# Kernel tuning notes

Measured on AMD Instinct MI355X. Metric: run time of the kernel, lower is better.

The kernel has to match this reference:

```python
import jax, jax.numpy as jnp
import numpy as np

N_NODES = 100000
N_EDGES = 800000
DIM = 64
HEADS = 4
HEAD_DIM = DIM // HEADS  # 16
ALPHA = 0.1
K_ITERS = 8  # fixed-point iterations approximating the implicit/CG solve


def setup_inputs() -> dict:
    key = jax.random.key(0)
    ks = jax.random.split(key, 7)
    x = jax.random.normal(ks[0], (N_NODES, DIM), dtype=jnp.float32)
    edge_index = jax.random.randint(ks[1], (2, N_EDGES), 0, N_NODES, dtype=jnp.int64)
    edge_attr = jax.random.normal(ks[2], (N_EDGES, DIM), dtype=jnp.float32)
    s = 1.0 / np.sqrt(DIM)
    Wq = jax.random.normal(ks[3], (DIM, DIM), dtype=jnp.float32) * s
    Wk = jax.random.normal(ks[4], (DIM, DIM), dtype=jnp.float32) * s
    Wv = jax.random.normal(ks[5], (DIM, DIM), dtype=jnp.float32) * s
    We = jax.random.normal(ks[6], (DIM, DIM), dtype=jnp.float32) * s
    return {"x": x, "edge_index": edge_index, "edge_attr": edge_attr,
            "Wq": Wq, "Wk": Wk, "Wv": Wv, "We": We}


def _mapr(x, edge_index, edge_attr, Wq, Wk, Wv, We):
    N = x.shape[0]
    src, dst = edge_index[0], edge_index[1]
    q = (x @ Wq).reshape(N, HEADS, HEAD_DIM)
    k = (x @ Wk).reshape(N, HEADS, HEAD_DIM)
    v = (x @ Wv).reshape(N, HEADS, HEAD_DIM)
    e = (edge_attr @ We).reshape(-1, HEADS, HEAD_DIM)
    # per-edge multi-head dot attention logits, edge features modulate keys
    logits = jnp.sum(q[dst] * (k[src] + e), axis=-1) / np.sqrt(HEAD_DIM)  # [E,H]
    # segment softmax over incoming edges of each dst node
    m = jax.ops.segment_max(logits, dst, num_segments=N)  # [N,H]
    ex = jnp.exp(logits - m[dst])
    denom = jax.ops.segment_sum(ex, dst, num_segments=N)  # [N,H]
    att = ex / (denom[dst] + 1e-16)  # [E,H]
    # implicit propagation: fixed-point solve of z = alpha*v + (1-alpha) * A_att z
    def step(z, _):
        msg = att[:, :, None] * z[src]                       # [E,H,D]
        agg = jax.ops.segment_sum(msg, dst, num_segments=N)  # [N,H,D]
        return ALPHA * v + (1.0 - ALPHA) * agg, None
    z, _ = jax.lax.scan(step, v, None, length=K_ITERS)
    return z.reshape(N, DIM)


def reference(x, edge_index, edge_attr, Wq, Wk, Wv, We):
    h = _mapr(x, edge_index, edge_attr, Wq, Wk, Wv, We)
    h = jax.nn.relu(h)  # act; dropout is identity in eval mode
    return x + h        # residual
```

## Files before the change

### kernel.cpp

```cpp
#include <hip/hip_runtime.h>
#include <hip/hip_fp16.h>
#include <cstdint>
#include <cstddef>

#define NN 100000
#define NE 800000
#define DIM 64
#define HEADS 4
#define HEAD_DIM 16
#define ALPHA 0.1f
#define K_ITERS 8
#define NBLK 391

typedef short bf16x8 __attribute__((ext_vector_type(8)));
typedef float f32x4 __attribute__((ext_vector_type(4)));

__device__ __forceinline__ unsigned short f2bf(float f) {
    unsigned int x = __float_as_uint(f);
    unsigned int r = (x + 0x7fffu + ((x >> 16) & 1u)) >> 16;
    return (unsigned short)r;
}
__device__ __forceinline__ float bf_lo(unsigned int p) { return __uint_as_float(p << 16); }
__device__ __forceinline__ float bf_hi(unsigned int p) { return __uint_as_float(p & 0xffff0000u); }

__device__ __forceinline__ float2 h2f(unsigned int v) {
    __half2 h = *(__half2*)&v;
    return __half22float2(h);
}
__device__ __forceinline__ unsigned int f2h2(float a, float b) {
    __half2 h = __floats2half2_rn(a, b);
    return *(unsigned int*)&h;
}
__device__ __forceinline__ float dot8h(uint4 a, uint4 b) {
    float2 a0 = h2f(a.x), b0 = h2f(b.x);
    float2 a1 = h2f(a.y), b1 = h2f(b.y);
    float2 a2 = h2f(a.z), b2 = h2f(b.z);
    float2 a3 = h2f(a.w), b3 = h2f(b.w);
    return a0.x * b0.x + a0.y * b0.y + a1.x * b1.x + a1.y * b1.y
         + a2.x * b2.x + a2.y * b2.y + a3.x * b3.x + a3.y * b3.y;
}

#define ACC8(a, V) { float2 t_; \
    t_ = h2f((V).x); m[0] += (a) * t_.x; m[1] += (a) * t_.y; \
    t_ = h2f((V).y); m[2] += (a) * t_.x; m[3] += (a) * t_.y; \
    t_ = h2f((V).z); m[4] += (a) * t_.x; m[5] += (a) * t_.y; \
    t_ = h2f((V).w); m[6] += (a) * t_.x; m[7] += (a) * t_.y; }

__global__ __launch_bounds__(256) void qkv_mfma_kernel(
    const float* __restrict__ x,
    const float* __restrict__ Wq, const float* __restrict__ Wk,
    const float* __restrict__ Wv, const float* __restrict__ We,
    __half* __restrict__ qh, __half* __restrict__ kh, __half* __restrict__ vh,
    unsigned short* __restrict__ u)
{
    __shared__ unsigned short sq[64 * 72];
    int tid = threadIdx.x;
    int w = tid >> 6;
    int lane = tid & 63;
    int m16 = lane & 15;
    int quad = lane >> 4;
    int node = blockIdx.x * 64 + w * 16 + m16;
    int nodeC = node < NN ? node : NN - 1;

    bf16x8 afrag[2];
    #pragma unroll
    for (int kk = 0; kk < 2; ++kk) {
        const float* xr = x + (size_t)nodeC * DIM + kk * 32 + quad * 8;
        #pragma unroll
        for (int j = 0; j < 8; ++j) afrag[kk][j] = (short)f2bf(xr[j]);
    }

    const float* Ws[3] = {Wq, Wk, Wv};
    __half* outs[3] = {qh, kh, vh};

    #pragma unroll
    for (int mtx = 0; mtx < 3; ++mtx) {
        const float* W = Ws[mtx];
        #pragma unroll
        for (int n0 = 0; n0 < 64; n0 += 16) {
            int col = n0 + m16;
            f32x4 acc = {0.f, 0.f, 0.f, 0.f};
            #pragma unroll
            for (int kk = 0; kk < 2; ++kk) {
                bf16x8 bfrag;
                #pragma unroll
                for (int j = 0; j < 8; ++j)
                    bfrag[j] = (short)f2bf(W[(kk * 32 + quad * 8 + j) * DIM + col]);
                acc = __builtin_amdgcn_mfma_f32_16x16x32_bf16(afrag[kk], bfrag, acc, 0, 0, 0);
            }
            if (mtx == 0) {
                #pragma unroll
                for (int r = 0; r < 4; ++r) acc[r] *= 0.25f;
            }
            #pragma unroll
            for (int r = 0; r < 4; ++r) {
                int rl = w * 16 + quad * 4 + r;
                int gnode = blockIdx.x * 64 + rl;
                if (mtx == 0) sq[rl * 72 + col] = f2bf(acc[r]);
                if (gnode < NN) outs[mtx][(size_t)gnode * DIM + col] = __float2half(acc[r]);
            }
        }
    }
    __syncthreads();

    #pragma unroll
    for (int h = 0; h < HEADS; ++h) {
        int kk = h >> 1;
        bf16x8 aq;
        const unsigned short* sr = &sq[(w * 16 + m16) * 72 + kk * 32 + quad * 8];
        #pragma unroll
        for (int j = 0; j < 8; ++j) aq[j] = (short)sr[j];
        #pragma unroll
        for (int c0 = 0; c0 < 64; c0 += 16) {
            int c = c0 + m16;
            bf16x8 bfrag;
            #pragma unroll
            for (int j = 0; j < 8; ++j) {
                int k = kk * 32 + quad * 8 + j;
                bfrag[j] = ((k >> 4) == h) ? (short)f2bf(We[c * DIM + k]) : (short)0;
            }
            f32x4 acc = {0.f, 0.f, 0.f, 0.f};
            acc = __builtin_amdgcn_mfma_f32_16x16x32_bf16(aq, bfrag, acc, 0, 0, 0);
            #pragma unroll
            for (int r = 0; r < 4; ++r) {
                int gnode = blockIdx.x * 64 + w * 16 + quad * 4 + r;
                if (gnode < NN) u[(size_t)gnode * 256 + h * 64 + c] = f2bf(acc[r]);
            }
        }
    }
}

__global__ void init_kernel(float* __restrict__ denom, int* __restrict__ deg) {
    int i = blockIdx.x * 256 + threadIdx.x;
    if (i < NN * HEADS) denom[i] = 0.f;
    if (i < NN) deg[i] = 0;
}

__global__ void deg_kernel(const int* __restrict__ ei, int* __restrict__ deg) {
    int e = blockIdx.x * 256 + threadIdx.x;
    if (e >= NE) return;
    atomicAdd(&deg[ei[NE + e]], 1);
}

__global__ void blocksum_kernel(const int* __restrict__ deg, int* __restrict__ bsum) {
    int t = threadIdx.x, b = blockIdx.x;
    int idx = b * 256 + t;
    int v = (idx < NN) ? deg[idx] : 0;
    #pragma unroll
    for (int off = 32; off > 0; off >>= 1) v += __shfl_down(v, off);
    __shared__ int wsum[4];
    if ((t & 63) == 0) wsum[t >> 6] = v;
    __syncthreads();
    if (t == 0) bsum[b] = wsum[0] + wsum[1] + wsum[2] + wsum[3];
}

__global__ void bscan_kernel(const int* __restrict__ bsum, int* __restrict__ boff) {
    __shared__ int s[512];
    int t = threadIdx.x;
    int v = (t < NBLK) ? bsum[t] : 0;
    s[t] = v;
    __syncthreads();
    for (int off = 1; off < 512; off <<= 1) {
        int u = (t >= off) ? s[t - off] : 0;
        __syncthreads();
        s[t] += u;
        __syncthreads();
    }
    if (t < NBLK) boff[t] = s[t] - v;
}

__global__ void rowptr_kernel(const int* __restrict__ deg, const int* __restrict__ boff,
                              int* __restrict__ row_ptr, int* __restrict__ cursor) {
    __shared__ int s[256];
    int t = threadIdx.x, b = blockIdx.x;
    int idx = b * 256 + t;
    int v = (idx < NN) ? deg[idx] : 0;
    s[t] = v;
    __syncthreads();
    for (int off = 1; off < 256; off <<= 1) {
        int u = (t >= off) ? s[t - off] : 0;
        __syncthreads();
        s[t] += u;
        __syncthreads();
    }
    if (idx < NN) {
        int ex = boff[b] + s[t] - v;
        row_ptr[idx] = ex;
        cursor[idx] = ex;
    }
    if (idx == 0) row_ptr[NN] = NE;
}

__global__ void scatter_kernel(const int* __restrict__ ei,
                               int* __restrict__ cursor,
                               int* __restrict__ csr_src,
                               int* __restrict__ csr_e,
                               int* __restrict__ csr_dst) {
    int e = blockIdx.x * 256 + threadIdx.x;
    if (e >= NE) return;
    int src = ei[e], dst = ei[NE + e];
    int pos = atomicAdd(&cursor[dst], 1);
    csr_src[pos] = src;
    csr_e[pos] = e;
    csr_dst[pos] = dst;
}

__global__ void logits_csr_kernel(const __half* __restrict__ qh,
                                  const __half* __restrict__ kh,
                                  const float* __restrict__ edge_attr,
                                  const unsigned short* __restrict__ u,
                                  const int* __restrict__ csr_src,
                                  const int* __restrict__ csr_e,
                                  const int* __restrict__ csr_dst,
                                  __half* __restrict__ att,
                                  float* __restrict__ denom) {
    int idx = blockIdx.x * 256 + threadIdx.x;
    if (idx >= NE * HEADS) return;
    int j = idx >> 2, h = idx & 3;
    int src = csr_src[j], dst = csr_dst[j], e = csr_e[j];
    const float4* attr4 = (const float4*)edge_attr + (size_t)e * 16;
    const uint4* u4 = (const uint4*)u + (size_t)dst * 32 + h * 8;
    float au = 0.f;
    #pragma unroll
    for (int i = 0; i < 8; ++i) {
        uint4 up = u4[i];
        float4 a0 = attr4[2 * i];
        float4 a1 = attr4[2 * i + 1];
        au += a0.x * bf_lo(up.x) + a0.y * bf_hi(up.x)
            + a0.z * bf_lo(up.y) + a0.w * bf_hi(up.y)
            + a1.x * bf_lo(up.z) + a1.y * bf_hi(up.z)
            + a1.z * bf_lo(up.w) + a1.w * bf_hi(up.w);
    }
    const uint4* qq = (const uint4*)qh + (size_t)dst * 8 + h * 2;
    const uint4* kk = (const uint4*)kh + (size_t)src * 8 + h * 2;
    float qk = dot8h(qq[0], kk[0]) + dot8h(qq[1], kk[1]);
    float ex = __expf(qk + au);
    att[idx] = __float2half(ex);
    atomicAdd(&denom[dst * HEADS + h], ex);
}

__global__ void prop_csr_kernel(const __half* __restrict__ zin,
                                const __half* __restrict__ vh,
                                const __half* __restrict__ att,
                                const int* __restrict__ csr_src,
                                const int* __restrict__ row_ptr,
                                const float* __restrict__ denom,
                                __half* __restrict__ zout) {
    int gid = blockIdx.x * 256 + threadIdx.x;
    int node = gid >> 3;
    if (node >= NN) return;
    int l = gid & 7;
    int head = l >> 1;
    const uint4* z4 = (const uint4*)zin;
    float m[8];
    #pragma unroll
    for (int i = 0; i < 8; ++i) m[i] = 0.f;
    int beg = row_ptr[node], end = row_ptr[node + 1];
    int j = beg;
    for (; j + 4 <= end; j += 4) {
        int s0 = csr_src[j], s1 = csr_src[j + 1], s2 = csr_src[j + 2], s3 = csr_src[j + 3];
        float a0 = __half2float(att[4 * j + head]);
        float a1 = __half2float(att[4 * j + 4 + head]);
        float a2 = __half2float(att[4 * j + 8 + head]);
        float a3 = __half2float(att[4 * j + 12 + head]);
        uint4 z0 = z4[(size_t)s0 * 8 + l];
        uint4 z1 = z4[(size_t)s1 * 8 + l];
        uint4 z2 = z4[(size_t)s2 * 8 + l];
        uint4 z3 = z4[(size_t)s3 * 8 + l];
        ACC8(a0, z0); ACC8(a1, z1); ACC8(a2, z2); ACC8(a3, z3);
    }
    for (; j < end; ++j) {
        int s = csr_src[j];
        float a = __half2float(att[4 * j + head]);
        uint4 zl = z4[(size_t)s * 8 + l];
        ACC8(a, zl);
    }
    float r = 0.9f / (denom[node * HEADS + head] + 1e-16f);
    uint4 vv = ((const uint4*)vh)[(size_t)node * 8 + l];
    float2 v0 = h2f(vv.x), v1 = h2f(vv.y), v2 = h2f(vv.z), v3 = h2f(vv.w);
    uint4 o;
    o.x = f2h2(ALPHA * v0.x + r * m[0], ALPHA * v0.y + r * m[1]);
    o.y = f2h2(ALPHA * v1.x + r * m[2], ALPHA * v1.y + r * m[3]);
    o.z = f2h2(ALPHA * v2.x + r * m[4], ALPHA * v2.y + r * m[5]);
    o.w = f2h2(ALPHA * v3.x + r * m[6], ALPHA * v3.y + r * m[7]);
    ((uint4*)zout)[(size_t)node * 8 + l] = o;
}

__global__ void prop_out_kernel(const __half* __restrict__ zin,
                                const __half* __restrict__ vh,
                                const __half* __restrict__ att,
                                const int* __restrict__ csr_src,
                                const int* __restrict__ row_ptr,
                                const float* __restrict__ denom,
                                const float* __restrict__ x,
                                float* __restrict__ out) {
    int gid = blockIdx.x * 256 + threadIdx.x;
    int node = gid >> 3;
    if (node >= NN) return;
    int l = gid & 7;
    int head = l >> 1;
    const uint4* z4 = (const uint4*)zin;
    float m[8];
    #pragma unroll
    for (int i = 0; i < 8; ++i) m[i] = 0.f;
    int beg = row_ptr[node], end = row_ptr[node + 1];
    int j = beg;
    for (; j + 4 <= end; j += 4) {
        int s0 = csr_src[j], s1 = csr_src[j + 1], s2 = csr_src[j + 2], s3 = csr_src[j + 3];
        float a0 = __half2float(att[4 * j + head]);
        float a1 = __half2float(att[4 * j + 4 + head]);
        float a2 = __half2float(att[4 * j + 8 + head]);
        float a3 = __half2float(att[4 * j + 12 + head]);
        uint4 z0 = z4[(size_t)s0 * 8 + l];
        uint4 z1 = z4[(size_t)s1 * 8 + l];
        uint4 z2 = z4[(size_t)s2 * 8 + l];
        uint4 z3 = z4[(size_t)s3 * 8 + l];
        ACC8(a0, z0); ACC8(a1, z1); ACC8(a2, z2); ACC8(a3, z3);
    }
    for (; j < end; ++j) {
        int s = csr_src[j];
        float a = __half2float(att[4 * j + head]);
        uint4 zl = z4[(size_t)s * 8 + l];
        ACC8(a, zl);
    }
    float r = 0.9f / (denom[node * HEADS + head] + 1e-16f);
    uint4 vv = ((const uint4*)vh)[(size_t)node * 8 + l];
    float2 v0 = h2f(vv.x), v1 = h2f(vv.y), v2 = h2f(vv.z), v3 = h2f(vv.w);
    float zf[8] = { ALPHA * v0.x + r * m[0], ALPHA * v0.y + r * m[1],
                    ALPHA * v1.x + r * m[2], ALPHA * v1.y + r * m[3],
                    ALPHA * v2.x + r * m[4], ALPHA * v2.y + r * m[5],
                    ALPHA * v3.x + r * m[6], ALPHA * v3.y + r * m[7] };
    const float4* x4 = (const float4*)x + (size_t)node * 16 + l * 2;
    float4 xa = x4[0], xb = x4[1];
    float4 oa, ob;
    oa.x = xa.x + fmaxf(zf[0], 0.f); oa.y = xa.y + fmaxf(zf[1], 0.f);
    oa.z = xa.z + fmaxf(zf[2], 0.f); oa.w = xa.w + fmaxf(zf[3], 0.f);
    ob.x = xb.x + fmaxf(zf[4], 0.f); ob.y = xb.y + fmaxf(zf[5], 0.f);
    ob.z = xb.z + fmaxf(zf[6], 0.f); ob.w = xb.w + fmaxf(zf[7], 0.f);
    float4* o4 = (float4*)out + (size_t)node * 16 + l * 2;
    o4[0] = oa; o4[1] = ob;
}

extern "C" void kernel_launch(void* const* d_in, const int* in_sizes, int n_in,
                              void* d_out, int out_size, void* d_ws, size_t ws_size,
                              hipStream_t stream) {
    const float* x         = (const float*)d_in[0];
    const int*   ei        = (const int*)d_in[1];
    const float* edge_attr = (const float*)d_in[2];
    const float* Wq        = (const float*)d_in[3];
    const float* Wk        = (const float*)d_in[4];
    const float* Wv        = (const float*)d_in[5];
    const float* We        = (const float*)d_in[6];
    float* out = (float*)d_out;

    __half* qh = (__half*)d_ws;
    __half* kh = qh + (size_t)NN * DIM;
    __half* vh = kh + (size_t)NN * DIM;
    unsigned short* u = (unsigned short*)(vh + (size_t)NN * DIM);
    __half* zha = (__half*)(u + (size_t)NN * 256);
    __half* zhb = zha + (size_t)NN * DIM;
    __half* att = zhb + (size_t)NN * DIM;
    float* denom = (float*)(att + (size_t)NE * HEADS);
    int* deg     = (int*)(denom + (size_t)NN * HEADS);
    int* bsum    = deg + NN;
    int* boff    = bsum + NBLK;
    int* row_ptr = boff + NBLK;
    int* cursor  = row_ptr + NN + 1;
    int* csr_src = cursor + NN;
    int* csr_e   = csr_src + NE;
    int* csr_dst = csr_e + NE;

    hipLaunchKernelGGL(qkv_mfma_kernel, dim3((NN + 63) / 64), dim3(256), 0, stream,
                       x, Wq, Wk, Wv, We, qh, kh, vh, u);
    hipLaunchKernelGGL(init_kernel, dim3((NN * HEADS + 255) / 256), dim3(256), 0, stream,
                       denom, deg);
    hipLaunchKernelGGL(deg_kernel, dim3((NE + 255) / 256), dim3(256), 0, stream,
                       ei, deg);
    hipLaunchKernelGGL(blocksum_kernel, dim3(NBLK), dim3(256), 0, stream,
                       deg, bsum);
    hipLaunchKernelGGL(bscan_kernel, dim3(1), dim3(512), 0, stream,
                       bsum, boff);
    hipLaunchKernelGGL(rowptr_kernel, dim3(NBLK), dim3(256), 0, stream,
                       deg, boff, row_ptr, cursor);
    hipLaunchKernelGGL(scatter_kernel, dim3((NE + 255) / 256), dim3(256), 0, stream,
                       ei, cursor, csr_src, csr_e, csr_dst);
    hipLaunchKernelGGL(logits_csr_kernel, dim3(NE * HEADS / 256), dim3(256), 0, stream,
                       qh, kh, edge_attr, u, csr_src, csr_e, csr_dst, att, denom);

    const __half* zin = vh;
    __half* zout = zha;
    for (int it = 0; it < K_ITERS - 1; ++it) {
        hipLaunchKernelGGL(prop_csr_kernel, dim3((NN * 8 + 255) / 256), dim3(256), 0, stream,
                           zin, vh, att, csr_src, row_ptr, denom, zout);
        zin = zout;
        zout = (zout == zha) ? zhb : zha;
    }
    hipLaunchKernelGGL(prop_out_kernel, dim3((NN * 8 + 255) / 256), dim3(256), 0, stream,
                       zin, vh, att, csr_src, row_ptr, denom, x, out);
}
```

Measured before the change: 734.9 us.

## Pack normalized attention and src into per-edge CSR records, drop denom atomics

Logits are now computed in original edge order, so edge_attr streams coalesced with nontemporal loads, and the per-edge atomicAdd into denom is removed. A per-node kernel sums the softmax denominator over CSR rows and stores a scaled reciprocal. A second kernel builds 16-byte CSR records holding src plus four pre-normalized half attention weights, which the eight propagation passes read with one vector load per edge. This adds two extra launches and a gathered read of att_e, and the normalized weights are now rounded to half.

```diff
diff --git a/kernel.cpp b/kernel.cpp
--- a/kernel.cpp
+++ b/kernel.cpp
@@ -14,6 +14,7 @@
 
 typedef short bf16x8 __attribute__((ext_vector_type(8)));
 typedef float f32x4 __attribute__((ext_vector_type(4)));
+typedef float fvec4 __attribute__((ext_vector_type(4)));
 
 __device__ __forceinline__ unsigned short f2bf(float f) {
     unsigned int x = __float_as_uint(f);
@@ -45,6 +46,12 @@
     t_ = h2f((V).y); m[2] += (a) * t_.x; m[3] += (a) * t_.y; \
     t_ = h2f((V).z); m[4] += (a) * t_.x; m[5] += (a) * t_.y; \
     t_ = h2f((V).w); m[6] += (a) * t_.x; m[7] += (a) * t_.y; }
+
+__device__ __forceinline__ float rec_att(uint4 r, int head) {
+    unsigned int pair = (head & 2) ? r.z : r.y;
+    float2 f = h2f(pair);
+    return (head & 1) ? f.y : f.x;
+}
 
 __global__ __launch_bounds__(256) void qkv_mfma_kernel(
     const float* __restrict__ x,
@@ -130,9 +137,8 @@
     }
 }
 
-__global__ void init_kernel(float* __restrict__ denom, int* __restrict__ deg) {
+__global__ void init_kernel(int* __restrict__ deg) {
     int i = blockIdx.x * 256 + threadIdx.x;
-    if (i < NN * HEADS) denom[i] = 0.f;
     if (i < NN) deg[i] = 0;
 }
 
@@ -205,27 +211,25 @@
     csr_dst[pos] = dst;
 }
 
-__global__ void logits_csr_kernel(const __half* __restrict__ qh,
-                                  const __half* __restrict__ kh,
-                                  const float* __restrict__ edge_attr,
-                                  const unsigned short* __restrict__ u,
-                                  const int* __restrict__ csr_src,
-                                  const int* __restrict__ csr_e,
-                                  const int* __restrict__ csr_dst,
-                                  __half* __restrict__ att,
-                                  float* __restrict__ denom) {
+__global__ __launch_bounds__(256) void logits_edge_kernel(
+    const __half* __restrict__ qh,
+    const __half* __restrict__ kh,
+    const float* __restrict__ edge_attr,
+    const unsigned short* __restrict__ u,
+    const int* __restrict__ ei,
+    __half* __restrict__ att_e) {
     int idx = blockIdx.x * 256 + threadIdx.x;
     if (idx >= NE * HEADS) return;
-    int j = idx >> 2, h = idx & 3;
-    int src = csr_src[j], dst = csr_dst[j], e = csr_e[j];
-    const float4* attr4 = (const float4*)edge_attr + (size_t)e * 16;
+    int e = idx >> 2, h = idx & 3;
+    int src = ei[e], dst = ei[NE + e];
+    const fvec4* attr4 = (const fvec4*)edge_attr + (size_t)e * 16;
     const uint4* u4 = (const uint4*)u + (size_t)dst * 32 + h * 8;
     float au = 0.f;
     #pragma unroll
     for (int i = 0; i < 8; ++i) {
         uint4 up = u4[i];
-        float4 a0 = attr4[2 * i];
-        float4 a1 = attr4[2 * i + 1];
+        fvec4 a0 = __builtin_nontemporal_load(attr4 + 2 * i);
+        fvec4 a1 = __builtin_nontemporal_load(attr4 + 2 * i + 1);
         au += a0.x * bf_lo(up.x) + a0.y * bf_hi(up.x)
             + a0.z * bf_lo(up.y) + a0.w * bf_hi(up.y)
             + a1.x * bf_lo(up.z) + a1.y * bf_hi(up.z)
@@ -235,17 +239,55 @@
     const uint4* kk = (const uint4*)kh + (size_t)src * 8 + h * 2;
     float qk = dot8h(qq[0], kk[0]) + dot8h(qq[1], kk[1]);
     float ex = __expf(qk + au);
-    att[idx] = __float2half(ex);
-    atomicAdd(&denom[dst * HEADS + h], ex);
-}
-
-__global__ void prop_csr_kernel(const __half* __restrict__ zin,
-                                const __half* __restrict__ vh,
-                                const __half* __restrict__ att,
-                                const int* __restrict__ csr_src,
-                                const int* __restrict__ row_ptr,
-                                const float* __restrict__ denom,
-                                __half* __restrict__ zout) {
+    att_e[idx] = __float2half(ex);
+}
+
+__global__ void rinv_kernel(const __half* __restrict__ att_e,
+                            const int* __restrict__ csr_e,
+                            const int* __restrict__ row_ptr,
+                            float* __restrict__ rinv) {
+    int idx = blockIdx.x * 256 + threadIdx.x;
+    if (idx >= NN * HEADS) return;
+    int n = idx >> 2, h = idx & 3;
+    int beg = row_ptr[n], end = row_ptr[n + 1];
+    float s = 0.f;
+    int j = beg;
+    for (; j + 2 <= end; j += 2) {
+        int e0 = csr_e[j], e1 = csr_e[j + 1];
+        float a0 = __half2float(att_e[e0 * 4 + h]);
+        float a1 = __half2float(att_e[e1 * 4 + h]);
+        s += a0 + a1;
+    }
+    if (j < end) s += __half2float(att_e[csr_e[j] * 4 + h]);
+    rinv[idx] = 0.9f / (s + 1e-16f);
+}
+
+__global__ void recs_kernel(const __half* __restrict__ att_e,
+                            const int* __restrict__ csr_src,
+                            const int* __restrict__ csr_e,
+                            const int* __restrict__ csr_dst,
+                            const float* __restrict__ rinv,
+                            uint4* __restrict__ recs) {
+    int j = blockIdx.x * 256 + threadIdx.x;
+    if (j >= NE) return;
+    int e = csr_e[j], src = csr_src[j], dst = csr_dst[j];
+    uint2 ap = *(const uint2*)(att_e + (size_t)e * 4);
+    float2 e01 = h2f(ap.x), e23 = h2f(ap.y);
+    float4 rv = *(const float4*)(rinv + (size_t)dst * 4);
+    uint4 rec;
+    rec.x = (unsigned int)src;
+    rec.y = f2h2(e01.x * rv.x, e01.y * rv.y);
+    rec.z = f2h2(e23.x * rv.z, e23.y * rv.w);
+    rec.w = 0u;
+    recs[j] = rec;
+}
+
+__global__ __launch_bounds__(256) void prop_rec_kernel(
+    const __half* __restrict__ zin,
+    const __half* __restrict__ vh,
+    const uint4* __restrict__ recs,
+    const int* __restrict__ row_ptr,
+    __half* __restrict__ zout) {
     int gid = blockIdx.x * 256 + threadIdx.x;
     int node = gid >> 3;
     if (node >= NN) return;
@@ -258,42 +300,38 @@
     int beg = row_ptr[node], end = row_ptr[node + 1];
     int j = beg;
     for (; j + 4 <= end; j += 4) {
-        int s0 = csr_src[j], s1 = csr_src[j + 1], s2 = csr_src[j + 2], s3 = csr_src[j + 3];
-        float a0 = __half2float(att[4 * j + head]);
-        float a1 = __half2float(att[4 * j + 4 + head]);
-        float a2 = __half2float(att[4 * j + 8 + head]);
-        float a3 = __half2float(att[4 * j + 12 + head]);
-        uint4 z0 = z4[(size_t)s0 * 8 + l];
-        uint4 z1 = z4[(size_t)s1 * 8 + l];
-        uint4 z2 = z4[(size_t)s2 * 8 + l];
-        uint4 z3 = z4[(size_t)s3 * 8 + l];
+        uint4 r0 = recs[j], r1 = recs[j + 1], r2 = recs[j + 2], r3 = recs[j + 3];
+        uint4 z0 = z4[(size_t)r0.x * 8 + l];
+        uint4 z1 = z4[(size_t)r1.x * 8 + l];
+        uint4 z2 = z4[(size_t)r2.x * 8 + l];
+        uint4 z3 = z4[(size_t)r3.x * 8 + l];
+        float a0 = rec_att(r0, head), a1 = rec_att(r1, head);
+        float a2 = rec_att(r2, head), a3 = rec_att(r3, head);
         ACC8(a0, z0); ACC8(a1, z1); ACC8(a2, z2); ACC8(a3, z3);
     }
     for (; j < end; ++j) {
-        int s = csr_src[j];
-        float a = __half2float(att[4 * j + head]);
-        uint4 zl = z4[(size_t)s * 8 + l];
+        uint4 r = recs[j];
+        uint4 zl = z4[(size_t)r.x * 8 + l];
+        float a = rec_att(r, head);
         ACC8(a, zl);
     }
-    float r = 0.9f / (denom[node * HEADS + head] + 1e-16f);
     uint4 vv = ((const uint4*)vh)[(size_t)node * 8 + l];
     float2 v0 = h2f(vv.x), v1 = h2f(vv.y), v2 = h2f(vv.z), v3 = h2f(vv.w);
     uint4 o;
-    o.x = f2h2(ALPHA * v0.x + r * m[0], ALPHA * v0.y + r * m[1]);
-    o.y = f2h2(ALPHA * v1.x + r * m[2], ALPHA * v1.y + r * m[3]);
-    o.z = f2h2(ALPHA * v2.x + r * m[4], ALPHA * v2.y + r * m[5]);
-    o.w = f2h2(ALPHA * v3.x + r * m[6], ALPHA * v3.y + r * m[7]);
+    o.x = f2h2(ALPHA * v0.x + m[0], ALPHA * v0.y + m[1]);
+    o.y = f2h2(ALPHA * v1.x + m[2], ALPHA * v1.y + m[3]);
+    o.z = f2h2(ALPHA * v2.x + m[4], ALPHA * v2.y + m[5]);
+    o.w = f2h2(ALPHA * v3.x + m[6], ALPHA * v3.y + m[7]);
     ((uint4*)zout)[(size_t)node * 8 + l] = o;
 }
 
-__global__ void prop_out_kernel(const __half* __restrict__ zin,
-                                const __half* __restrict__ vh,
-                                const __half* __restrict__ att,
-                                const int* __restrict__ csr_src,
-                                const int* __restrict__ row_ptr,
-                                const float* __restrict__ denom,
-                                const float* __restrict__ x,
-                                float* __restrict__ out) {
+__global__ __launch_bounds__(256) void prop_out_rec_kernel(
+    const __half* __restrict__ zin,
+    const __half* __restrict__ vh,
+    const uint4* __restrict__ recs,
+    const int* __restrict__ row_ptr,
+    const float* __restrict__ x,
+    float* __restrict__ out) {
     int gid = blockIdx.x * 256 + threadIdx.x;
     int node = gid >> 3;
     if (node >= NN) return;
@@ -306,30 +344,27 @@
     int beg = row_ptr[node], end = row_ptr[node + 1];
     int j = beg;
     for (; j + 4 <= end; j += 4) {
-        int s0 = csr_src[j], s1 = csr_src[j + 1], s2 = csr_src[j + 2], s3 = csr_src[j + 3];
-        float a0 = __half2float(att[4 * j + head]);
-        float a1 = __half2float(att[4 * j + 4 + head]);
-        float a2 = __half2float(att[4 * j + 8 + head]);
-        float a3 = __half2float(att[4 * j + 12 + head]);
-        uint4 z0 = z4[(size_t)s0 * 8 + l];
-        uint4 z1 = z4[(size_t)s1 * 8 + l];
-        uint4 z2 = z4[(size_t)s2 * 8 + l];
-        uint4 z3 = z4[(size_t)s3 * 8 + l];
+        uint4 r0 = recs[j], r1 = recs[j + 1], r2 = recs[j + 2], r3 = recs[j + 3];
+        uint4 z0 = z4[(size_t)r0.x * 8 + l];
+        uint4 z1 = z4[(size_t)r1.x * 8 + l];
+        uint4 z2 = z4[(size_t)r2.x * 8 + l];
+        uint4 z3 = z4[(size_t)r3.x * 8 + l];
+        float a0 = rec_att(r0, head), a1 = rec_att(r1, head);
+        float a2 = rec_att(r2, head), a3 = rec_att(r3, head);
         ACC8(a0, z0); ACC8(a1, z1); ACC8(a2, z2); ACC8(a3, z3);
     }
     for (; j < end; ++j) {
-        int s = csr_src[j];
-        float a = __half2float(att[4 * j + head]);
-        uint4 zl = z4[(size_t)s * 8 + l];
+        uint4 r = recs[j];
+        uint4 zl = z4[(size_t)r.x * 8 + l];
+        float a = rec_att(r, head);
         ACC8(a, zl);
     }
-    float r = 0.9f / (denom[node * HEADS + head] + 1e-16f);
     uint4 vv = ((const uint4*)vh)[(size_t)node * 8 + l];
     float2 v0 = h2f(vv.x), v1 = h2f(vv.y), v2 = h2f(vv.z), v3 = h2f(vv.w);
-    float zf[8] = { ALPHA * v0.x + r * m[0], ALPHA * v0.y + r * m[1],
-                    ALPHA * v1.x + r * m[2], ALPHA * v1.y + r * m[3],
-                    ALPHA * v2.x + r * m[4], ALPHA * v2.y + r * m[5],
-                    ALPHA * v3.x + r * m[6], ALPHA * v3.y + r * m[7] };
+    float zf[8] = { ALPHA * v0.x + m[0], ALPHA * v0.y + m[1],
+                    ALPHA * v1.x + m[2], ALPHA * v1.y + m[3],
+                    ALPHA * v2.x + m[4], ALPHA * v2.y + m[5],
+                    ALPHA * v3.x + m[6], ALPHA * v3.y + m[7] };
     const float4* x4 = (const float4*)x + (size_t)node * 16 + l * 2;
     float4 xa = x4[0], xb = x4[1];
     float4 oa, ob;
@@ -359,9 +394,10 @@
     unsigned short* u = (unsigned short*)(vh + (size_t)NN * DIM);
     __half* zha = (__half*)(u + (size_t)NN * 256);
     __half* zhb = zha + (size_t)NN * DIM;
-    __half* att = zhb + (size_t)NN * DIM;
-    float* denom = (float*)(att + (size_t)NE * HEADS);
-    int* deg     = (int*)(denom + (size_t)NN * HEADS);
+    __half* att_e = zhb + (size_t)NN * DIM;
+    float* rinv  = (float*)(att_e + (size_t)NE * HEADS);
+    uint4* recs  = (uint4*)(rinv + (size_t)NN * HEADS);
+    int* deg     = (int*)(recs + (size_t)NE);
     int* bsum    = deg + NN;
     int* boff    = bsum + NBLK;
     int* row_ptr = boff + NBLK;
@@ -372,8 +408,8 @@
 
     hipLaunchKernelGGL(qkv_mfma_kernel, dim3((NN + 63) / 64), dim3(256), 0, stream,
                        x, Wq, Wk, Wv, We, qh, kh, vh, u);
-    hipLaunchKernelGGL(init_kernel, dim3((NN * HEADS + 255) / 256), dim3(256), 0, stream,
-                       denom, deg);
+    hipLaunchKernelGGL(init_kernel, dim3((NN + 255) / 256), dim3(256), 0, stream,
+                       deg);
     hipLaunchKernelGGL(deg_kernel, dim3((NE + 255) / 256), dim3(256), 0, stream,
                        ei, deg);
     hipLaunchKernelGGL(blocksum_kernel, dim3(NBLK), dim3(256), 0, stream,
@@ -384,17 +420,21 @@
                        deg, boff, row_ptr, cursor);
     hipLaunchKernelGGL(scatter_kernel, dim3((NE + 255) / 256), dim3(256), 0, stream,
                        ei, cursor, csr_src, csr_e, csr_dst);
-    hipLaunchKernelGGL(logits_csr_kernel, dim3(NE * HEADS / 256), dim3(256), 0, stream,
-                       qh, kh, edge_attr, u, csr_src, csr_e, csr_dst, att, denom);
+    hipLaunchKernelGGL(logits_edge_kernel, dim3(NE * HEADS / 256), dim3(256), 0, stream,
+                       qh, kh, edge_attr, u, ei, att_e);
+    hipLaunchKernelGGL(rinv_kernel, dim3((NN * HEADS + 255) / 256), dim3(256), 0, stream,
+                       att_e, csr_e, row_ptr, rinv);
+    hipLaunchKernelGGL(recs_kernel, dim3((NE + 255) / 256), dim3(256), 0, stream,
+                       att_e, csr_src, csr_e, csr_dst, rinv, recs);
 
     const __half* zin = vh;
     __half* zout = zha;
     for (int it = 0; it < K_ITERS - 1; ++it) {
-        hipLaunchKernelGGL(prop_csr_kernel, dim3((NN * 8 + 255) / 256), dim3(256), 0, stream,
-                           zin, vh, att, csr_src, row_ptr, denom, zout);
+        hipLaunchKernelGGL(prop_rec_kernel, dim3((NN * 8 + 255) / 256), dim3(256), 0, stream,
+                           zin, vh, recs, row_ptr, zout);
         zin = zout;
         zout = (zout == zha) ? zhb : zha;
     }
-    hipLaunchKernelGGL(prop_out_kernel, dim3((NN * 8 + 255) / 256), dim3(256), 0, stream,
-                       zin, vh, att, csr_src, row_ptr, denom, x, out);
-}
+    hipLaunchKernelGGL(prop_out_rec_kernel, dim3((NN * 8 + 255) / 256), dim3(256), 0, stream,
+                       zin, vh, recs, row_ptr, x, out);
+}
```

Measured after the change: 847.4 us. +15.3%, slower.
